# Optimization experiments

Measured on AMD Instinct MI355X. Metric: run time of the kernel, lower is better.

Reference implementation:

```python
import jax, jax.numpy as jnp
import numpy as np

T, D, H, E, K = 4096, 2048, 1408, 8, 2  # tokens, d_model, d_intermediate, n_experts, top_k


def setup_inputs() -> dict:
    key = jax.random.key(0)
    ks = jax.random.split(key, 5)
    x = jax.random.normal(ks[0], (T, D), dtype=jnp.float32)
    # distinct top-k expert ids per token (router output)
    indices = jnp.argsort(jax.random.uniform(ks[1], (T, E)), axis=-1)[:, :K].astype(jnp.int32)
    w = jax.random.uniform(ks[2], (T, K), dtype=jnp.float32) + 0.1
    weights = w / jnp.sum(w, axis=-1, keepdims=True)
    # stacked expert params: fc1 [E, 2H, D], fc2 [E, D, H] (nn.Linear layout)
    w1 = jax.random.normal(ks[3], (E, 2 * H, D), dtype=jnp.float32) * (D ** -0.5)
    w2 = jax.random.normal(ks[4], (E, D, H), dtype=jnp.float32) * (H ** -0.5)
    return {"x": x, "weights": weights, "indices": indices, "w1": w1, "w2": w2}


def reference(x, weights, indices, w1, w2):
    # combine weight per (expert, token): sum of routing weights where token routed to expert e
    onehot = jax.nn.one_hot(indices, E, dtype=x.dtype)          # [T, K, E]
    cw = jnp.einsum('tk,tke->et', weights, onehot)              # [E, T]

    def body(y, inp):
        w1_i, w2_i, cw_i = inp
        h = x @ w1_i.T                                          # [T, 2H]
        u, g = jnp.split(h, 2, axis=-1)                         # value, gate (chunk order of GatedMLP)
        out = (u * jax.nn.silu(g)) @ w2_i.T                     # [T, D]
        return y + out * cw_i[:, None], None

    y, _ = jax.lax.scan(body, jnp.zeros_like(x), (w1, w2, cw))
    return y
```

## Files before the change

### kernel.cpp

```cpp
#include <hip/hip_runtime.h>
#include <stdint.h>

#define T_TOK 4096
#define DMODEL 2048
#define HDIM 1408
#define NEXP 8
#define TOPK 2

#define BM 128
#define BN 128
#define BK 64
#define MAX_TILES ((T_TOK * TOPK) / BM + NEXP)

typedef unsigned short u16;
typedef __bf16 bf16x8 __attribute__((ext_vector_type(8)));
typedef float f32x4 __attribute__((ext_vector_type(4)));

__device__ __forceinline__ u16 f2bf(float f) {
  union { float f; uint32_t u; } v; v.f = f;
  uint32_t r = (v.u + 0x7FFFu + ((v.u >> 16) & 1u)) >> 16;
  return (u16)r;
}

__device__ __forceinline__ void gll16(const void* g, void* l) {
  __builtin_amdgcn_global_load_lds(
      (__attribute__((address_space(1))) void*)(uintptr_t)g,
      (__attribute__((address_space(3))) void*)l, 16, 0, 0);
}

__global__ __launch_bounds__(256) void convert_all(
    const float* __restrict__ x, const float* __restrict__ w1,
    const float* __restrict__ w2, u16* __restrict__ xb,
    u16* __restrict__ w1b, u16* __restrict__ w2b) {
  const long c0 = (long)T_TOK * DMODEL / 8;
  const long c1 = (long)NEXP * 2 * HDIM * DMODEL / 8;
  const long c2 = (long)NEXP * DMODEL * HDIM / 8;
  const long total = c0 + c1 + c2;
  const long stride = (long)gridDim.x * blockDim.x;
  for (long i = blockIdx.x * (long)blockDim.x + threadIdx.x; i < total; i += stride) {
    const float* s; u16* d; long j;
    if (i < c0)            { s = x;  d = xb;  j = i; }
    else if (i < c0 + c1)  { s = w1; d = w1b; j = i - c0; }
    else                   { s = w2; d = w2b; j = i - c0 - c1; }
    const float4* sp = (const float4*)s + j * 2;
    float4 v0 = sp[0], v1 = sp[1];
    union { u16 us[8]; uint4 u4; } o;
    o.us[0] = f2bf(v0.x); o.us[1] = f2bf(v0.y); o.us[2] = f2bf(v0.z); o.us[3] = f2bf(v0.w);
    o.us[4] = f2bf(v1.x); o.us[5] = f2bf(v1.y); o.us[6] = f2bf(v1.z); o.us[7] = f2bf(v1.w);
    *((uint4*)(d + j * 8)) = o.u4;
  }
}

__global__ void route_kernel(const int* __restrict__ idx, int* __restrict__ cnt,
                             int* __restrict__ perm) {
  int i = blockIdx.x * blockDim.x + threadIdx.x;
  if (i < T_TOK * TOPK) {
    int e = idx[i];
    int p = atomicAdd(&cnt[e], 1);
    perm[e * T_TOK + p] = i;
  }
}

__global__ void tilemap_kernel(const int* __restrict__ cnt, int* __restrict__ tmap,
                               int* __restrict__ ntp) {
  if (threadIdx.x == 0 && blockIdx.x == 0) {
    int nt = 0;
    for (int e = 0; e < NEXP; ++e) {
      int n = cnt[e];
      for (int r = 0; r < n; r += BM) tmap[nt++] = (e << 16) | r;
    }
    *ntp = nt;
  }
}

template <int MODE>
__global__ __launch_bounds__(256, 2) void moe_gemm(
    const u16* __restrict__ A, const u16* __restrict__ Bw,
    const float* __restrict__ wts, const int* __restrict__ perm,
    const int* __restrict__ cnt, const int* __restrict__ tmap,
    const int* __restrict__ ntp, u16* __restrict__ act,
    float* __restrict__ pairs) {
  constexpr int KD = (MODE == 0) ? DMODEL : HDIM;
  if ((int)blockIdx.x >= *ntp) return;
  const int tm = tmap[blockIdx.x];
  const int e = tm >> 16, r0 = tm & 0xFFFF;
  const int ne = cnt[e];

  __shared__ int rid_s[BM];
  __shared__ __align__(16) u16 Asm[BM][BK];
  __shared__ __align__(16) u16 Bu[BM][BK];
  __shared__ __align__(16) u16 Bg[(MODE == 0) ? BM : 1][BK];

  const int tid = threadIdx.x;
  if (tid < BM) {
    int ii = r0 + tid;
    rid_s[tid] = perm[e * T_TOK + (ii < ne ? ii : ne - 1)];
  }
  __syncthreads();

  const int wave = tid >> 6;
  const int lane = tid & 63;
  const int wr = wave >> 1, wc = wave & 1;

  const int col8 = (tid & 7) * 8;
  const u16* aptr[4];
  const u16* buptr[4];
  const u16* bgptr[4];
#pragma unroll
  for (int r = 0; r < 4; ++r) {
    int row = (tid >> 3) + r * 32;
    int rid = rid_s[row];
    long arow = (MODE == 0) ? (long)(rid >> 1) : (long)rid;
    aptr[r] = A + arow * KD + col8;
    if constexpr (MODE == 0) {
      buptr[r] = Bw + ((long)e * 2 * HDIM + blockIdx.y * BN + row) * KD + col8;
      bgptr[r] = Bw + ((long)e * 2 * HDIM + HDIM + blockIdx.y * BN + row) * KD + col8;
    } else {
      buptr[r] = Bw + ((long)e * DMODEL + blockIdx.y * BN + row) * KD + col8;
    }
  }
  char* aldst = (char*)(&Asm[0][0]) + wave * 1024;
  char* buldst = (char*)(&Bu[0][0]) + wave * 1024;
  char* bgldst = (char*)(&Bg[0][0]) + wave * 1024;

  f32x4 accU[4][4] = {};
  f32x4 accG[4][4] = {};

  for (int k0 = 0; k0 < KD; k0 += BK) {
    __syncthreads();
#pragma unroll
    for (int r = 0; r < 4; ++r) {
      gll16(aptr[r] + k0, aldst + r * 4096);
      gll16(buptr[r] + k0, buldst + r * 4096);
      if constexpr (MODE == 0) gll16(bgptr[r] + k0, bgldst + r * 4096);
    }
    __syncthreads();
#pragma unroll
    for (int ks = 0; ks < 2; ++ks) {
      const int koff = ks * 32 + (lane >> 4) * 8;
      const int rsel = lane & 15;
      bf16x8 a[4], bu[4], bg[4];
#pragma unroll
      for (int m = 0; m < 4; ++m)
        a[m] = *(const bf16x8*)&Asm[wr * 64 + m * 16 + rsel][koff];
#pragma unroll
      for (int n = 0; n < 4; ++n) {
        bu[n] = *(const bf16x8*)&Bu[wc * 64 + n * 16 + rsel][koff];
        if constexpr (MODE == 0)
          bg[n] = *(const bf16x8*)&Bg[wc * 64 + n * 16 + rsel][koff];
      }
#pragma unroll
      for (int m = 0; m < 4; ++m)
#pragma unroll
        for (int n = 0; n < 4; ++n) {
          accU[m][n] = __builtin_amdgcn_mfma_f32_16x16x32_bf16(a[m], bu[n], accU[m][n], 0, 0, 0);
          if constexpr (MODE == 0)
            accG[m][n] = __builtin_amdgcn_mfma_f32_16x16x32_bf16(a[m], bg[n], accG[m][n], 0, 0, 0);
        }
    }
  }

  const int cbase = blockIdx.y * BN + wc * 64;
#pragma unroll
  for (int m = 0; m < 4; ++m) {
    const int rb = wr * 64 + m * 16 + (lane >> 4) * 4;
#pragma unroll
    for (int rg = 0; rg < 4; ++rg) {
      const int rloc = rb + rg;
      if (r0 + rloc >= ne) continue;
      const int rid = rid_s[rloc];
      if constexpr (MODE == 0) {
#pragma unroll
        for (int n = 0; n < 4; ++n) {
          const int col = cbase + n * 16 + (lane & 15);
          float g = accG[m][n][rg];
          float u = accU[m][n][rg];
          float val = u * (g / (1.f + __expf(-g)));
          act[(long)rid * HDIM + col] = f2bf(val);
        }
      } else {
        const float w = wts[rid];
#pragma unroll
        for (int n = 0; n < 4; ++n) {
          const int col = cbase + n * 16 + (lane & 15);
          pairs[(long)rid * DMODEL + col] = accU[m][n][rg] * w;
        }
      }
    }
  }
}

__global__ __launch_bounds__(256) void reduce_pairs(const float* __restrict__ pairs,
                                                    float* __restrict__ y) {
  const long total = (long)T_TOK * DMODEL / 4;
  const long stride = (long)gridDim.x * blockDim.x;
  for (long i = blockIdx.x * (long)blockDim.x + threadIdx.x; i < total; i += stride) {
    long t = (i * 4) / DMODEL;
    long d = (i * 4) % DMODEL;
    float4 a = *(const float4*)(pairs + (2 * t) * DMODEL + d);
    float4 b = *(const float4*)(pairs + (2 * t + 1) * DMODEL + d);
    float4 r;
    r.x = a.x + b.x; r.y = a.y + b.y; r.z = a.z + b.z; r.w = a.w + b.w;
    *(float4*)(y + t * DMODEL + d) = r;
  }
}

extern "C" void kernel_launch(void* const* d_in, const int* in_sizes, int n_in,
                              void* d_out, int out_size, void* d_ws, size_t ws_size,
                              hipStream_t stream) {
  const float* x = (const float*)d_in[0];
  const float* wts = (const float*)d_in[1];
  const int* idx = (const int*)d_in[2];
  const float* w1 = (const float*)d_in[3];
  const float* w2 = (const float*)d_in[4];
  float* y = (float*)d_out;

  char* ws = (char*)d_ws;
  size_t off = 0;
  int* cnt = (int*)(ws + off); off += 256;
  int* ntp = (int*)(ws + off); off += 256;
  int* tmap = (int*)(ws + off); off += 1024;
  int* perm = (int*)(ws + off); off += (size_t)NEXP * T_TOK * 4;
  off = (off + 255) & ~(size_t)255;
  size_t xb_off = off;
  u16* xb = (u16*)(ws + off);  off += (size_t)T_TOK * DMODEL * 2;
  u16* w1b = (u16*)(ws + off); off += (size_t)NEXP * 2 * HDIM * DMODEL * 2;
  u16* w2b = (u16*)(ws + off); off += (size_t)NEXP * DMODEL * HDIM * 2;
  u16* act = (u16*)(ws + off); off += (size_t)T_TOK * TOPK * HDIM * 2;
  float* pairs = (float*)(ws + xb_off);

  hipMemsetAsync(cnt, 0, 256, stream);
  convert_all<<<2048, 256, 0, stream>>>(x, w1, w2, xb, w1b, w2b);
  route_kernel<<<(T_TOK * TOPK + 255) / 256, 256, 0, stream>>>(idx, cnt, perm);
  tilemap_kernel<<<1, 64, 0, stream>>>(cnt, tmap, ntp);
  moe_gemm<0><<<dim3(MAX_TILES, HDIM / BN), 256, 0, stream>>>(
      xb, w1b, wts, perm, cnt, tmap, ntp, act, nullptr);
  moe_gemm<1><<<dim3(MAX_TILES, DMODEL / BN), 256, 0, stream>>>(
      act, w2b, wts, perm, cnt, tmap, ntp, nullptr, pairs);
  reduce_pairs<<<2048, 256, 0, stream>>>(pairs, y);
}
```

Measured before the change: 666.8 us.

## Use 256x256 tiles with a 4-stage LDS pipeline and swizzled loads in the MoE GEMMs

The grouped GEMM moves to 512-thread blocks with 256x256 output tiles and BK=32. It uses a 4-deep ring of dynamic-LDS buffers filled by global_load_lds, with explicit vmcnt waits, barriers and setprio to overlap the loads with MFMA work. LDS addresses are XOR-swizzled to avoid bank conflicts. In the gated fc1 kernel, the up and gate rows share one B tile, and the gate half is exchanged through LDS in the epilogue so the other waves can apply SiLU. The larger tiles raise arithmetic intensity and reduce barrier stalls, at the cost of more padding waste on partial expert tiles, higher register pressure, and 129KB of LDS per block, which limits occupancy.

```diff
diff --git a/kernel.cpp b/kernel.cpp
--- a/kernel.cpp
+++ b/kernel.cpp
@@ -7,10 +7,11 @@
 #define NEXP 8
 #define TOPK 2
 
-#define BM 128
-#define BN 128
-#define BK 64
-#define MAX_TILES ((T_TOK * TOPK) / BM + NEXP)
+#define BM 256
+#define BN 256
+#define BK 32
+#define MAX_TILES (T_TOK * TOPK / BM + NEXP)
+#define SMEM_BYTES (131072 + 1024)
 
 typedef unsigned short u16;
 typedef __bf16 bf16x8 __attribute__((ext_vector_type(8)));
@@ -73,24 +74,53 @@
   }
 }
 
+
+template <int H, int VMN>
+__device__ __forceinline__ void phase_core(const char* bc, const int (&aoffR)[8],
+                                           const int (&boffR)[4], f32x4 (&acc)[8][4]) {
+  bf16x8 a_[4], b_[4];
+#pragma unroll
+  for (int m = 0; m < 4; ++m) a_[m] = *(const bf16x8*)(bc + aoffR[H * 4 + m]);
+#pragma unroll
+  for (int n = 0; n < 4; ++n) b_[n] = *(const bf16x8*)(bc + boffR[n]);
+  if constexpr (VMN == 8) {
+    asm volatile("s_waitcnt vmcnt(8)" ::: "memory");
+    __builtin_amdgcn_sched_barrier(0);
+  } else if constexpr (VMN == 4) {
+    asm volatile("s_waitcnt vmcnt(4)" ::: "memory");
+    __builtin_amdgcn_sched_barrier(0);
+  } else if constexpr (VMN == 0) {
+    asm volatile("s_waitcnt vmcnt(0)" ::: "memory");
+    __builtin_amdgcn_sched_barrier(0);
+  }
+  __builtin_amdgcn_s_barrier();
+  __builtin_amdgcn_s_setprio(1);
+#pragma unroll
+  for (int m = 0; m < 4; ++m)
+#pragma unroll
+    for (int n = 0; n < 4; ++n)
+      acc[H * 4 + m][n] = __builtin_amdgcn_mfma_f32_16x16x32_bf16(
+          a_[m], b_[n], acc[H * 4 + m][n], 0, 0, 0);
+  __builtin_amdgcn_s_setprio(0);
+  __builtin_amdgcn_s_barrier();
+}
+
 template <int MODE>
-__global__ __launch_bounds__(256, 2) void moe_gemm(
+__global__ __launch_bounds__(512, 2) void moe_gemm(
     const u16* __restrict__ A, const u16* __restrict__ Bw,
     const float* __restrict__ wts, const int* __restrict__ perm,
     const int* __restrict__ cnt, const int* __restrict__ tmap,
     const int* __restrict__ ntp, u16* __restrict__ act,
     float* __restrict__ pairs) {
   constexpr int KD = (MODE == 0) ? DMODEL : HDIM;
+  constexpr int NT = KD / BK;
+  extern __shared__ char smem[];
+  int* rid_s = (int*)(smem + 131072);
+
   if ((int)blockIdx.x >= *ntp) return;
   const int tm = tmap[blockIdx.x];
   const int e = tm >> 16, r0 = tm & 0xFFFF;
   const int ne = cnt[e];
-
-  __shared__ int rid_s[BM];
-  __shared__ __align__(16) u16 Asm[BM][BK];
-  __shared__ __align__(16) u16 Bu[BM][BK];
-  __shared__ __align__(16) u16 Bg[(MODE == 0) ? BM : 1][BK];
-
   const int tid = threadIdx.x;
   if (tid < BM) {
     int ii = r0 + tid;
@@ -98,92 +128,138 @@
   }
   __syncthreads();
 
-  const int wave = tid >> 6;
-  const int lane = tid & 63;
-  const int wr = wave >> 1, wc = wave & 1;
-
-  const int col8 = (tid & 7) * 8;
-  const u16* aptr[4];
-  const u16* buptr[4];
-  const u16* bgptr[4];
-#pragma unroll
-  for (int r = 0; r < 4; ++r) {
-    int row = (tid >> 3) + r * 32;
-    int rid = rid_s[row];
-    long arow = (MODE == 0) ? (long)(rid >> 1) : (long)rid;
-    aptr[r] = A + arow * KD + col8;
-    if constexpr (MODE == 0) {
-      buptr[r] = Bw + ((long)e * 2 * HDIM + blockIdx.y * BN + row) * KD + col8;
-      bgptr[r] = Bw + ((long)e * 2 * HDIM + HDIM + blockIdx.y * BN + row) * KD + col8;
-    } else {
-      buptr[r] = Bw + ((long)e * DMODEL + blockIdx.y * BN + row) * KD + col8;
-    }
-  }
-  char* aldst = (char*)(&Asm[0][0]) + wave * 1024;
-  char* buldst = (char*)(&Bu[0][0]) + wave * 1024;
-  char* bgldst = (char*)(&Bg[0][0]) + wave * 1024;
-
-  f32x4 accU[4][4] = {};
-  f32x4 accG[4][4] = {};
-
-  for (int k0 = 0; k0 < KD; k0 += BK) {
-    __syncthreads();
-#pragma unroll
-    for (int r = 0; r < 4; ++r) {
-      gll16(aptr[r] + k0, aldst + r * 4096);
-      gll16(buptr[r] + k0, buldst + r * 4096);
-      if constexpr (MODE == 0) gll16(bgptr[r] + k0, bgldst + r * 4096);
+  const int w = tid >> 6, l = tid & 63;
+  const int wr = w >> 2, wc = w & 3;
+  const int yb = blockIdx.y;
+
+  const int ar1 = 32 * w + (l >> 2);
+  const int ar2 = ar1 + 16;
+  const int sslot = ((l & 3) ^ ((l >> 3) & 3)) * 8;
+  long arow1, arow2;
+  {
+    int rid1 = rid_s[ar1], rid2 = rid_s[ar2];
+    arow1 = (MODE == 0) ? (rid1 >> 1) : rid1;
+    arow2 = (MODE == 0) ? (rid2 >> 1) : rid2;
+  }
+  const u16* aptr1 = A + arow1 * KD + sslot;
+  const u16* aptr2 = A + arow2 * KD + sslot;
+  long brow1, brow2;
+  if constexpr (MODE == 0) {
+    brow1 = (long)e * (2 * HDIM) + (ar1 < 128 ? yb * 128 + ar1 : HDIM + yb * 128 + ar1 - 128);
+    brow2 = (long)e * (2 * HDIM) + (ar2 < 128 ? yb * 128 + ar2 : HDIM + yb * 128 + ar2 - 128);
+  } else {
+    brow1 = (long)e * DMODEL + yb * BN + ar1;
+    brow2 = (long)e * DMODEL + yb * BN + ar2;
+  }
+  const u16* bptr1 = Bw + brow1 * KD + sslot;
+  const u16* bptr2 = Bw + brow2 * KD + sslot;
+  const int aoffL1 = 2 * w * 1024, aoffL2 = aoffL1 + 1024;
+  const int boffL1 = 16384 + 2 * w * 1024, boffL2 = boffL1 + 1024;
+
+  const int swz = ((l >> 4) ^ ((l >> 1) & 3)) * 16;
+  int aoffR[8];
+#pragma unroll
+  for (int h = 0; h < 2; ++h)
+#pragma unroll
+    for (int m = 0; m < 4; ++m)
+      aoffR[h * 4 + m] = (wr * 128 + h * 64 + m * 16 + (l & 15)) * 64 + swz;
+  int boffR[4];
+#pragma unroll
+  for (int n = 0; n < 4; ++n)
+    boffR[n] = 16384 + (wc * 64 + n * 16 + (l & 15)) * 64 + swz;
+
+  f32x4 acc[8][4] = {};
+
+#pragma unroll
+  for (int tt = 0; tt < 3; ++tt) {
+    char* sb = smem + tt * 32768;
+    const size_t kq = (size_t)tt * BK;
+    gll16(aptr1 + kq, sb + aoffL1);
+    gll16(aptr2 + kq, sb + aoffL2);
+    gll16(bptr1 + kq, sb + boffL1);
+    gll16(bptr2 + kq, sb + boffL2);
+  }
+  asm volatile("s_waitcnt vmcnt(8)" ::: "memory");
+  __builtin_amdgcn_sched_barrier(0);
+  __builtin_amdgcn_s_barrier();
+
+  for (int t = 0; t <= NT - 4; ++t) {
+    const char* bufc = smem + (t & 3) * 32768;
+    char* sb = smem + ((t + 3) & 3) * 32768;
+    const size_t kq = (size_t)(t + 3) * BK;
+    gll16(aptr1 + kq, sb + aoffL1);
+    gll16(aptr2 + kq, sb + aoffL2);
+    phase_core<0, -1>(bufc, aoffR, boffR, acc);
+    gll16(bptr1 + kq, sb + boffL1);
+    gll16(bptr2 + kq, sb + boffL2);
+    phase_core<1, 8>(bufc, aoffR, boffR, acc);
+  }
+  {
+    const char* bufc = smem + ((NT - 3) & 3) * 32768;
+    phase_core<0, -1>(bufc, aoffR, boffR, acc);
+    phase_core<1, 4>(bufc, aoffR, boffR, acc);
+  }
+  {
+    const char* bufc = smem + ((NT - 2) & 3) * 32768;
+    phase_core<0, -1>(bufc, aoffR, boffR, acc);
+    phase_core<1, 0>(bufc, aoffR, boffR, acc);
+  }
+  {
+    const char* bufc = smem + ((NT - 1) & 3) * 32768;
+    phase_core<0, -1>(bufc, aoffR, boffR, acc);
+    phase_core<1, -1>(bufc, aoffR, boffR, acc);
+  }
+
+  if constexpr (MODE == 0) {
+    float* g_lds = (float*)smem;
+    if (wc >= 2) {
+      const int cl = (wc - 2) * 64;
+#pragma unroll
+      for (int mm = 0; mm < 8; ++mm)
+#pragma unroll
+        for (int n = 0; n < 4; ++n)
+#pragma unroll
+          for (int rg = 0; rg < 4; ++rg) {
+            int row = wr * 128 + mm * 16 + (l >> 4) * 4 + rg;
+            g_lds[row * 128 + cl + n * 16 + (l & 15)] = acc[mm][n][rg];
+          }
     }
     __syncthreads();
-#pragma unroll
-    for (int ks = 0; ks < 2; ++ks) {
-      const int koff = ks * 32 + (lane >> 4) * 8;
-      const int rsel = lane & 15;
-      bf16x8 a[4], bu[4], bg[4];
-#pragma unroll
-      for (int m = 0; m < 4; ++m)
-        a[m] = *(const bf16x8*)&Asm[wr * 64 + m * 16 + rsel][koff];
-#pragma unroll
-      for (int n = 0; n < 4; ++n) {
-        bu[n] = *(const bf16x8*)&Bu[wc * 64 + n * 16 + rsel][koff];
-        if constexpr (MODE == 0)
-          bg[n] = *(const bf16x8*)&Bg[wc * 64 + n * 16 + rsel][koff];
+    if (wc < 2) {
+      const int cl = wc * 64;
+#pragma unroll
+      for (int mm = 0; mm < 8; ++mm) {
+        const int rb = wr * 128 + mm * 16 + (l >> 4) * 4;
+#pragma unroll
+        for (int rg = 0; rg < 4; ++rg) {
+          const int rloc = rb + rg;
+          if (r0 + rloc >= ne) continue;
+          const int rid = rid_s[rloc];
+#pragma unroll
+          for (int n = 0; n < 4; ++n) {
+            const int col = cl + n * 16 + (l & 15);
+            float g = g_lds[rloc * 128 + col];
+            float u = acc[mm][n][rg];
+            float val = u * (g / (1.f + __expf(-g)));
+            act[(size_t)rid * HDIM + yb * 128 + col] = f2bf(val);
+          }
+        }
       }
-#pragma unroll
-      for (int m = 0; m < 4; ++m)
+    }
+  } else {
+#pragma unroll
+    for (int mm = 0; mm < 8; ++mm) {
+      const int rb = wr * 128 + mm * 16 + (l >> 4) * 4;
+#pragma unroll
+      for (int rg = 0; rg < 4; ++rg) {
+        const int rloc = rb + rg;
+        if (r0 + rloc >= ne) continue;
+        const int rid = rid_s[rloc];
+        const float wt = wts[rid];
 #pragma unroll
         for (int n = 0; n < 4; ++n) {
-          accU[m][n] = __builtin_amdgcn_mfma_f32_16x16x32_bf16(a[m], bu[n], accU[m][n], 0, 0, 0);
-          if constexpr (MODE == 0)
-            accG[m][n] = __builtin_amdgcn_mfma_f32_16x16x32_bf16(a[m], bg[n], accG[m][n], 0, 0, 0);
-        }
-    }
-  }
-
-  const int cbase = blockIdx.y * BN + wc * 64;
-#pragma unroll
-  for (int m = 0; m < 4; ++m) {
-    const int rb = wr * 64 + m * 16 + (lane >> 4) * 4;
-#pragma unroll
-    for (int rg = 0; rg < 4; ++rg) {
-      const int rloc = rb + rg;
-      if (r0 + rloc >= ne) continue;
-      const int rid = rid_s[rloc];
-      if constexpr (MODE == 0) {
-#pragma unroll
-        for (int n = 0; n < 4; ++n) {
-          const int col = cbase + n * 16 + (lane & 15);
-          float g = accG[m][n][rg];
-          float u = accU[m][n][rg];
-          float val = u * (g / (1.f + __expf(-g)));
-          act[(long)rid * HDIM + col] = f2bf(val);
-        }
-      } else {
-        const float w = wts[rid];
-#pragma unroll
-        for (int n = 0; n < 4; ++n) {
-          const int col = cbase + n * 16 + (lane & 15);
-          pairs[(long)rid * DMODEL + col] = accU[m][n][rg] * w;
+          const int col = yb * BN + wc * 64 + n * 16 + (l & 15);
+          pairs[(size_t)rid * DMODEL + col] = acc[mm][n][rg] * wt;
         }
       }
     }
@@ -229,13 +305,18 @@
   u16* act = (u16*)(ws + off); off += (size_t)T_TOK * TOPK * HDIM * 2;
   float* pairs = (float*)(ws + xb_off);
 
+  (void)hipFuncSetAttribute((const void*)moe_gemm<0>,
+                            hipFuncAttributeMaxDynamicSharedMemorySize, SMEM_BYTES);
+  (void)hipFuncSetAttribute((const void*)moe_gemm<1>,
+                            hipFuncAttributeMaxDynamicSharedMemorySize, SMEM_BYTES);
+
   hipMemsetAsync(cnt, 0, 256, stream);
   convert_all<<<2048, 256, 0, stream>>>(x, w1, w2, xb, w1b, w2b);
   route_kernel<<<(T_TOK * TOPK + 255) / 256, 256, 0, stream>>>(idx, cnt, perm);
   tilemap_kernel<<<1, 64, 0, stream>>>(cnt, tmap, ntp);
-  moe_gemm<0><<<dim3(MAX_TILES, HDIM / BN), 256, 0, stream>>>(
+  moe_gemm<0><<<dim3(MAX_TILES, HDIM / 128), 512, SMEM_BYTES, stream>>>(
       xb, w1b, wts, perm, cnt, tmap, ntp, act, nullptr);
-  moe_gemm<1><<<dim3(MAX_TILES, DMODEL / BN), 256, 0, stream>>>(
+  moe_gemm<1><<<dim3(MAX_TILES, DMODEL / BN), 512, SMEM_BYTES, stream>>>(
       act, w2b, wts, perm, cnt, tmap, ntp, nullptr, pairs);
   reduce_pairs<<<2048, 256, 0, stream>>>(pairs, y);
 }
```

After: 642.1 us. -3.7%, faster.
